# Optimization experiments

Measured on AMD Instinct MI355X. Metric: run time of the kernel, lower is better.

## Reference

```python
import jax, jax.numpy as jnp
import numpy as np

CROP_H = 7
CROP_W = 7
EXTRAP = 0.0  # module hardcodes 0 when calling CropAndResizeFunction


def _crop_and_resize(image, boxes, box_ind):
    """TF-style crop_and_resize.
    image: (N,C,H,W) float; boxes: (M,4) normalized (y1,x1,y2,x2); box_ind: (M,) int32.
    Returns (M,C,CROP_H,CROP_W).
    """
    N, C, H, W = image.shape
    dt = image.dtype
    y1, x1, y2, x2 = boxes[:, 0], boxes[:, 1], boxes[:, 2], boxes[:, 3]
    ii = jnp.arange(CROP_H, dtype=dt)
    jj = jnp.arange(CROP_W, dtype=dt)
    # sample coordinates in feature-map space, shape (M, CROP_H) / (M, CROP_W)
    y = y1[:, None] * (H - 1) + ii[None, :] * ((y2 - y1) * (H - 1) / (CROP_H - 1))[:, None]
    x = x1[:, None] * (W - 1) + jj[None, :] * ((x2 - x1) * (W - 1) / (CROP_W - 1))[:, None]
    valid_y = (y >= 0) & (y <= H - 1)
    valid_x = (x >= 0) & (x <= W - 1)
    yt_f = jnp.floor(y)
    xt_f = jnp.floor(x)
    y_lerp = y - yt_f  # (M, oh)
    x_lerp = x - xt_f  # (M, ow)
    yt = jnp.clip(yt_f, 0, H - 1).astype(jnp.int32)
    yb = jnp.clip(jnp.ceil(y), 0, H - 1).astype(jnp.int32)
    xl = jnp.clip(xt_f, 0, W - 1).astype(jnp.int32)
    xr = jnp.clip(jnp.ceil(x), 0, W - 1).astype(jnp.int32)
    img = jnp.transpose(image, (0, 2, 3, 1))  # (N,H,W,C) for clean gather
    b = box_ind[:, None, None]                # (M,1,1)
    tl = img[b, yt[:, :, None], xl[:, None, :]]  # (M,oh,ow,C)
    tr = img[b, yt[:, :, None], xr[:, None, :]]
    bl = img[b, yb[:, :, None], xl[:, None, :]]
    br = img[b, yb[:, :, None], xr[:, None, :]]
    xl_w = x_lerp[:, None, :, None]
    top = tl + (tr - tl) * xl_w
    bot = bl + (br - bl) * xl_w
    out = top + (bot - top) * y_lerp[:, :, None, None]
    valid = (valid_y[:, :, None] & valid_x[:, None, :])[..., None]
    out = jnp.where(valid, out, jnp.asarray(EXTRAP, dt))
    return jnp.transpose(out, (0, 3, 1, 2))  # (M,C,oh,ow)


def setup_inputs() -> dict:
    key = jax.random.key(0)
    k0, k1, k2, k3, k4, k5 = jax.random.split(key, 6)
    N, C, H, W = 2, 256, 200, 304
    M = 2048
    scale = 0.0625  # 1/16
    Himg, Wimg = H / scale, W / scale
    featuremap = jax.random.normal(k0, (N, C, H, W), dtype=jnp.float32)
    x1 = jax.random.uniform(k1, (M, 1), minval=0.0, maxval=Wimg - 260.0)
    y1 = jax.random.uniform(k2, (M, 1), minval=0.0, maxval=Himg - 260.0)
    bw = jax.random.uniform(k3, (M, 1), minval=32.0, maxval=256.0)
    bh = jax.random.uniform(k4, (M, 1), minval=32.0, maxval=256.0)
    ids = jax.random.randint(k5, (M, 1), 0, N).astype(jnp.float32)
    rois = jnp.concatenate([ids, x1, y1, x1 + bw, y1 + bh], axis=1)
    return {"featuremap": featuremap, "rois": rois, "spatial_scale": jnp.float32(scale)}


def reference(featuremap, rois, spatial_scale):
    H, W = featuremap.shape[2], featuremap.shape[3]
    boxes = rois[:, 1:5] * spatial_scale
    box_ind = rois[:, 0].astype(jnp.int32)
    x1, y1, x2, y2 = boxes[:, 0], boxes[:, 1], boxes[:, 2], boxes[:, 3]
    spacing_w = (x2 - x1) / CROP_W
    spacing_h = (y2 - y1) / CROP_H
    nx0 = (x1 + spacing_w / 2 - 0.5) / (W - 1)
    ny0 = (y1 + spacing_h / 2 - 0.5) / (H - 1)
    nw = spacing_w * (CROP_W - 1) / (W - 1)
    nh = spacing_h * (CROP_H - 1) / (H - 1)
    boxes_n = jnp.stack([ny0, nx0, ny0 + nh, nx0 + nw], axis=1)
    return _crop_and_resize(featuremap, boxes_n, box_ind)
```

## Files before the change

kernel.cpp:

```cpp
#include <hip/hip_runtime.h>

#define RA_C   256
#define RA_H   200
#define RA_W   304
#define RA_HW  (RA_H * RA_W)
#define RA_CHW (RA_C * RA_HW)
#define CROPN  7
#define CROP2  (CROPN * CROPN)
#define OUT_M  (RA_C * CROP2)
#define BC     8
#define BM     32
#define PER_BLK (BM * BC * CROP2)

__global__ __launch_bounds__(256) void roialign_kernel(
    const float* __restrict__ fm, const float* __restrict__ rois,
    const float* __restrict__ scale_p, float* __restrict__ out)
{
    __shared__ int   s_offT[BM][CROPN], s_offB[BM][CROPN];
    __shared__ float s_ylerp[BM][CROPN], s_vy[BM][CROPN];
    __shared__ int   s_xl[BM][CROPN], s_xr[BM][CROPN];
    __shared__ float s_xlerp[BM][CROPN], s_vx[BM][CROPN];
    __shared__ int   s_imgbase[BM];

    const int t = threadIdx.x;

    const int bid   = blockIdx.x;
    const int numBG = gridDim.x >> 5;
    const int xcd   = bid & 7;
    const int r     = bid >> 3;
    const int cgl   = r / numBG;
    const int bg    = r - cgl * numBG;
    const int c0    = (xcd * 4 + cgl) * BC;
    const int m0    = bg * BM;

    for (int task = t; task < BM * 2 * CROPN; task += 256) {
        #pragma clang fp contract(off)
        {
            const int mm  = task / (2 * CROPN);
            const int k14 = task - mm * (2 * CROPN);
            const int axis = (k14 >= CROPN) ? 1 : 0;
            const int k = axis ? (k14 - CROPN) : k14;
            const float scale = scale_p[0];
            const float* rr = rois + (size_t)(m0 + mm) * 5;
            if (k14 == 0) s_imgbase[mm] = (int)rr[0] * RA_CHW;
            float lo, hi, szm1;
            if (axis == 0) { lo = rr[2] * scale; hi = rr[4] * scale; szm1 = (float)(RA_H - 1); }
            else           { lo = rr[1] * scale; hi = rr[3] * scale; szm1 = (float)(RA_W - 1); }
            float sp   = (hi - lo) / 7.0f;
            float n0   = (lo + sp * 0.5f - 0.5f) / szm1;
            float nsz  = sp * 6.0f / szm1;
            float b2   = n0 + nsz;
            float d    = (b2 - n0) * szm1 / 6.0f;
            float coord = n0 * szm1 + (float)k * d;
            float fl = floorf(coord);
            float ce = ceilf(coord);
            float lerp = coord - fl;
            int lo_i = (int)fminf(fmaxf(fl, 0.0f), szm1);
            int hi_i = (int)fminf(fmaxf(ce, 0.0f), szm1);
            float valid = (coord >= 0.0f && coord <= szm1) ? 1.0f : 0.0f;
            if (axis == 0) {
                s_offT[mm][k] = lo_i * RA_W; s_offB[mm][k] = hi_i * RA_W;
                s_ylerp[mm][k] = lerp; s_vy[mm][k] = valid;
            } else {
                s_xl[mm][k] = lo_i; s_xr[mm][k] = hi_i;
                s_xlerp[mm][k] = lerp; s_vx[mm][k] = valid;
            }
        }
    }
    __syncthreads();

    for (int e = t; e < PER_BLK; e += 256) {
        int mm  = e / (BC * CROP2);
        int rem = e - mm * (BC * CROP2);
        int cc  = rem / CROP2;
        int ij  = rem - cc * CROP2;
        int i   = ij / CROPN;
        int j   = ij - i * CROPN;
        const float* __restrict__ p =
            fm + (size_t)s_imgbase[mm] + (size_t)(c0 + cc) * RA_HW;
        const int ot = s_offT[mm][i], ob = s_offB[mm][i];
        const int xl = s_xl[mm][j],  xr = s_xr[mm][j];
        const float xw = s_xlerp[mm][j];
        const float yw = s_ylerp[mm][i];
        const float v  = s_vy[mm][i] * s_vx[mm][j];
        float tl = p[ot + xl];
        float tr = p[ot + xr];
        float bl = p[ob + xl];
        float br = p[ob + xr];
        float top = tl + (tr - tl) * xw;
        float bot = bl + (br - bl) * xw;
        float res = (top + (bot - top) * yw) * v;
        out[(size_t)(m0 + mm) * OUT_M + (size_t)(c0 + cc) * CROP2 + ij] = res;
    }
}

extern "C" void kernel_launch(void* const* d_in, const int* in_sizes, int n_in,
                              void* d_out, int out_size, void* d_ws, size_t ws_size,
                              hipStream_t stream) {
    const float* fm    = (const float*)d_in[0];
    const float* rois  = (const float*)d_in[1];
    const float* scale = (const float*)d_in[2];
    float* out = (float*)d_out;
    const int M = in_sizes[1] / 5;
    const int numBG = M / BM;
    roialign_kernel<<<dim3(32 * numBG), dim3(256), 0, stream>>>(fm, rois, scale, out);
}
```

Before: 294.4 us.

## Map one wavefront per ROI and batch channel loads per thread

Shrinks the ROI tile per block from 32 to 4 so there are many more blocks. Each 64-lane wavefront now handles one ROI, with each lane owning one output pixel. Each thread computes its four gather addresses once and issues all 32 loads for 8 channels up front, which removes per-element index division and increases memory-level parallelism. The trade-off is 15 idle lanes per wavefront (64 lanes for 49 pixels) and extra per-block setup, including shared-memory coordinate computation for fewer ROIs.

```diff
diff --git a/kernel.cpp b/kernel.cpp
--- a/kernel.cpp
+++ b/kernel.cpp
@@ -9,8 +9,7 @@
 #define CROP2  (CROPN * CROPN)
 #define OUT_M  (RA_C * CROP2)
 #define BC     8
-#define BM     32
-#define PER_BLK (BM * BC * CROP2)
+#define BM     4
 
 __global__ __launch_bounds__(256) void roialign_kernel(
     const float* __restrict__ fm, const float* __restrict__ rois,
@@ -33,11 +32,11 @@
     const int c0    = (xcd * 4 + cgl) * BC;
     const int m0    = bg * BM;
 
-    for (int task = t; task < BM * 2 * CROPN; task += 256) {
+    if (t < BM * 2 * CROPN) {
         #pragma clang fp contract(off)
         {
-            const int mm  = task / (2 * CROPN);
-            const int k14 = task - mm * (2 * CROPN);
+            const int mm  = t / (2 * CROPN);
+            const int k14 = t - mm * (2 * CROPN);
             const int axis = (k14 >= CROPN) ? 1 : 0;
             const int k = axis ? (k14 - CROPN) : k14;
             const float scale = scale_p[0];
@@ -69,28 +68,39 @@
     }
     __syncthreads();
 
-    for (int e = t; e < PER_BLK; e += 256) {
-        int mm  = e / (BC * CROP2);
-        int rem = e - mm * (BC * CROP2);
-        int cc  = rem / CROP2;
-        int ij  = rem - cc * CROP2;
-        int i   = ij / CROPN;
-        int j   = ij - i * CROPN;
-        const float* __restrict__ p =
-            fm + (size_t)s_imgbase[mm] + (size_t)(c0 + cc) * RA_HW;
-        const int ot = s_offT[mm][i], ob = s_offB[mm][i];
-        const int xl = s_xl[mm][j],  xr = s_xr[mm][j];
-        const float xw = s_xlerp[mm][j];
-        const float yw = s_ylerp[mm][i];
-        const float v  = s_vy[mm][i] * s_vx[mm][j];
-        float tl = p[ot + xl];
-        float tr = p[ot + xr];
-        float bl = p[ob + xl];
-        float br = p[ob + xr];
-        float top = tl + (tr - tl) * xw;
-        float bot = bl + (br - bl) * xw;
-        float res = (top + (bot - top) * yw) * v;
-        out[(size_t)(m0 + mm) * OUT_M + (size_t)(c0 + cc) * CROP2 + ij] = res;
+    const int mm  = t >> 6;
+    const int ij  = t & 63;
+    const int ijc = (ij < CROP2) ? ij : (CROP2 - 1);
+    const int i   = ijc / CROPN;
+    const int j   = ijc - i * CROPN;
+
+    const float* __restrict__ img = fm + s_imgbase[mm] + (size_t)c0 * RA_HW;
+    const int aTL = s_offT[mm][i] + s_xl[mm][j];
+    const int aTR = s_offT[mm][i] + s_xr[mm][j];
+    const int aBL = s_offB[mm][i] + s_xl[mm][j];
+    const int aBR = s_offB[mm][i] + s_xr[mm][j];
+    const float xw = s_xlerp[mm][j];
+    const float yw = s_ylerp[mm][i];
+    const float vv = s_vy[mm][i] * s_vx[mm][j];
+
+    float tl[BC], tr[BC], bl[BC], br[BC];
+    #pragma unroll
+    for (int cc = 0; cc < BC; ++cc) {
+        const float* __restrict__ p = img + (size_t)cc * RA_HW;
+        tl[cc] = p[aTL];
+        tr[cc] = p[aTR];
+        bl[cc] = p[aBL];
+        br[cc] = p[aBR];
+    }
+    if (ij < CROP2) {
+        float* __restrict__ op =
+            out + (size_t)(m0 + mm) * OUT_M + (size_t)c0 * CROP2 + ij;
+        #pragma unroll
+        for (int cc = 0; cc < BC; ++cc) {
+            float top = tl[cc] + (tr[cc] - tl[cc]) * xw;
+            float bot = bl[cc] + (br[cc] - bl[cc]) * xw;
+            op[cc * CROP2] = (top + (bot - top) * yw) * vv;
+        }
     }
 }
 
```

Result: faster. 273.4 us (-7.1%).
